# Performance work log

Measured on AMD Instinct MI355X. Metric: run time of the kernel, lower is better.

Reference implementation:

```python
import jax, jax.numpy as jnp
import numpy as np

N = 50000   # nodes
E = 800000  # edges
C = 64      # num_channels
EPS = 1e-5


def setup_inputs() -> dict:
    key = jax.random.key(0)
    ks = jax.random.split(key, 12)
    x = jax.random.normal(ks[0], (N, C), dtype=jnp.float32)
    vec = jax.random.normal(ks[1], (N, 3, C), dtype=jnp.float32)
    senders = jax.random.randint(ks[2], (E,), 0, N, dtype=jnp.int32)
    receivers = jax.random.randint(ks[3], (E,), 0, N, dtype=jnp.int32)
    interaction_matrices = jax.random.normal(ks[4], (E, 3, 3), dtype=jnp.float32)
    # learned parameters
    ln_scale = jnp.ones((C,), dtype=jnp.float32)
    ln_bias = jnp.zeros((C,), dtype=jnp.float32)
    vln_weight = jnp.ones((C,), dtype=jnp.float32)  # VecLayerNorm weight (norm_type='none' -> identity norm, channel scale)
    w1 = jax.random.normal(ks[5], (C, 2 * C), dtype=jnp.float32) / np.sqrt(C)
    b1 = jnp.zeros((2 * C,), dtype=jnp.float32)
    w2 = jax.random.normal(ks[6], (2 * C, C), dtype=jnp.float32) / np.sqrt(2 * C)
    b2 = jnp.zeros((C,), dtype=jnp.float32)
    return {
        "x": x, "vec": vec, "senders": senders, "receivers": receivers,
        "interaction_matrices": interaction_matrices,
        "ln_scale": ln_scale, "ln_bias": ln_bias, "vln_weight": vln_weight,
        "w1": w1, "b1": b1, "w2": w2, "b2": b2,
    }


def reference(x, vec, senders, receivers, interaction_matrices,
              ln_scale, ln_bias, vln_weight, w1, b1, w2, b2):
    # LayerNorm(eps=1e-5) over channel dim
    mean = jnp.mean(x, axis=-1, keepdims=True)
    var = jnp.var(x, axis=-1, keepdims=True)
    x_norm = (x - mean) * jax.lax.rsqrt(var + EPS) * ln_scale + ln_bias
    # VecLayerNorm with norm_type='none': identity norm, learned per-channel weight
    vec_norm = vec * vln_weight  # [N, 3, C]
    # MLP: Dense(2C) -> silu -> Dense(C)
    p = jax.nn.silu(x_norm @ w1 + b1) @ w2 + b2  # [N, C]
    # gather to edges
    p_i = p[receivers]            # [E, C]
    p_j = p[senders]              # [E, C]
    vec_i = vec_norm[receivers]   # [E, 3, C]
    vec_j = vec_norm[senders]     # [E, 3, C]
    source_dipole = p_j[:, None, :] * vec_j                              # [E, 3, C]
    field_at_i = jnp.einsum('eij,ejc->eic', interaction_matrices, source_dipole)  # [E, 3, C]
    dEnergy = jnp.sum(p_i[:, None, :] * vec_i * field_at_i, axis=1)      # [E, C]
    dx = jax.ops.segment_sum(dEnergy, receivers, num_segments=x.shape[0])  # [N, C]
    return dx
```

## Files before the change

kernel.cpp:

```cpp
#include <hip/hip_runtime.h>

#define C 64
#define EPS 1e-5f

typedef __attribute__((ext_vector_type(8))) short bf16x8;
typedef __attribute__((ext_vector_type(4))) float f32x4;

static __device__ __forceinline__ unsigned int f2bf(float f) {
  unsigned int x = __float_as_uint(f);
  return (x + 0x7fffu + ((x >> 16) & 1u)) >> 16;
}
static __device__ __forceinline__ float bflo2f(unsigned int p) {
  return __uint_as_float(p << 16);
}
static __device__ __forceinline__ float bfhi2f(unsigned int p) {
  return __uint_as_float(p & 0xffff0000u);
}

__global__ __launch_bounds__(256) void prep_weights(
    const float* __restrict__ w1, const float* __restrict__ w2,
    unsigned short* __restrict__ w1T, unsigned short* __restrict__ w2T) {
  int idx = blockIdx.x * 256 + threadIdx.x;
  if (idx < 2 * C * C) {
    int k = idx >> 6, c = idx & 63;
    w1T[idx] = (unsigned short)f2bf(w1[c * 2 * C + k]);
  } else if (idx < 4 * C * C) {
    int j = idx - 2 * C * C;
    int c = j >> 7, k = j & 127;
    w2T[j] = (unsigned short)f2bf(w2[k * C + c]);
  }
}

__global__ __launch_bounds__(256, 2) void node_kernel(
    const float* __restrict__ x, const float* __restrict__ vec,
    const float* __restrict__ ln_scale, const float* __restrict__ ln_bias,
    const float* __restrict__ vln_w,
    const unsigned short* __restrict__ w1T, const float* __restrict__ b1,
    const unsigned short* __restrict__ w2T, const float* __restrict__ b2,
    uint2* __restrict__ D16, int n_nodes) {
  __shared__ unsigned short An[64 * 72];
  __shared__ unsigned short Ss[64 * 136];
  __shared__ unsigned short W1s[128 * 72];
  __shared__ unsigned short W2s[64 * 136];

  const int t = threadIdx.x;
  const int lane = t & 63;
  const int wave = t >> 6;
  const int l15 = lane & 15;
  const int q = lane >> 4;

  {
    int r1 = t >> 1, h2 = t & 1;
    const uint4* s1 = (const uint4*)(w1T + r1 * 64 + h2 * 32);
    uint4* d1 = (uint4*)(W1s + r1 * 72 + h2 * 32);
    d1[0] = s1[0]; d1[1] = s1[1]; d1[2] = s1[2]; d1[3] = s1[3];
    int r2 = t >> 2, qd = t & 3;
    const uint4* s2 = (const uint4*)(w2T + r2 * 128 + qd * 32);
    uint4* d2 = (uint4*)(W2s + r2 * 136 + qd * 32);
    d2[0] = s2[0]; d2[1] = s2[1]; d2[2] = s2[2]; d2[3] = s2[3];
  }

  {
    int rowl = t >> 2;
    int part = t & 3;
    int node = blockIdx.x * 64 + rowl;
    int nc = node < n_nodes ? node : n_nodes - 1;
    const float* xp = x + (size_t)nc * C + part * 16;
    float xv[16];
    float s = 0.f;
#pragma unroll
    for (int i = 0; i < 4; i++) {
      float4 v = *(const float4*)(xp + i * 4);
      xv[i * 4 + 0] = v.x; xv[i * 4 + 1] = v.y;
      xv[i * 4 + 2] = v.z; xv[i * 4 + 3] = v.w;
      s += v.x + v.y + v.z + v.w;
    }
    s += __shfl_xor(s, 1);
    s += __shfl_xor(s, 2);
    float mean = s * (1.f / C);
    float vs = 0.f;
#pragma unroll
    for (int i = 0; i < 16; i++) {
      float d = xv[i] - mean;
      vs += d * d;
    }
    vs += __shfl_xor(vs, 1);
    vs += __shfl_xor(vs, 2);
    float rs = rsqrtf(vs * (1.f / C) + EPS);
    float ls[16], lb[16];
#pragma unroll
    for (int i = 0; i < 4; i++) {
      float4 a = *(const float4*)(ln_scale + part * 16 + i * 4);
      float4 b = *(const float4*)(ln_bias + part * 16 + i * 4);
      ls[i * 4 + 0] = a.x; ls[i * 4 + 1] = a.y; ls[i * 4 + 2] = a.z; ls[i * 4 + 3] = a.w;
      lb[i * 4 + 0] = b.x; lb[i * 4 + 1] = b.y; lb[i * 4 + 2] = b.z; lb[i * 4 + 3] = b.w;
    }
    unsigned int bp[8];
#pragma unroll
    for (int i = 0; i < 8; i++) {
      float e0 = (xv[2 * i] - mean) * rs * ls[2 * i] + lb[2 * i];
      float e1 = (xv[2 * i + 1] - mean) * rs * ls[2 * i + 1] + lb[2 * i + 1];
      bp[i] = f2bf(e0) | (f2bf(e1) << 16);
    }
    uint4* dst = (uint4*)(An + rowl * 72 + part * 16);
    uint4 p0 = {bp[0], bp[1], bp[2], bp[3]};
    uint4 p1 = {bp[4], bp[5], bp[6], bp[7]};
    dst[0] = p0;
    dst[1] = p1;
  }
  __syncthreads();

  const int Mbase = wave * 16;

  bf16x8 a0 = *(const bf16x8*)(An + (Mbase + l15) * 72 + q * 8);
  bf16x8 a1 = *(const bf16x8*)(An + (Mbase + l15) * 72 + 32 + q * 8);
  f32x4 acc1[8];
#pragma unroll
  for (int nt = 0; nt < 8; nt++) {
    const unsigned short* wb = W1s + (nt * 16 + l15) * 72 + q * 8;
    bf16x8 b0 = *(const bf16x8*)(wb);
    bf16x8 b1f = *(const bf16x8*)(wb + 32);
    f32x4 z = {0.f, 0.f, 0.f, 0.f};
    z = __builtin_amdgcn_mfma_f32_16x16x32_bf16(a0, b0, z, 0, 0, 0);
    z = __builtin_amdgcn_mfma_f32_16x16x32_bf16(a1, b1f, z, 0, 0, 0);
    acc1[nt] = z;
  }
#pragma unroll
  for (int nt = 0; nt < 8; nt++) {
    float bb = b1[nt * 16 + l15];
#pragma unroll
    for (int r = 0; r < 4; r++) {
      float h = acc1[nt][r] + bb;
      float sg = h / (1.f + __expf(-h));
      Ss[(Mbase + q * 4 + r) * 136 + nt * 16 + l15] = (unsigned short)f2bf(sg);
    }
  }
  __syncthreads();

  bf16x8 a2[4];
#pragma unroll
  for (int kt = 0; kt < 4; kt++)
    a2[kt] = *(const bf16x8*)(Ss + (Mbase + l15) * 136 + kt * 32 + q * 8);
  f32x4 acc2[4];
#pragma unroll
  for (int nt = 0; nt < 4; nt++) {
    f32x4 z = {0.f, 0.f, 0.f, 0.f};
#pragma unroll
    for (int kt = 0; kt < 4; kt++) {
      bf16x8 b = *(const bf16x8*)(W2s + (nt * 16 + l15) * 136 + kt * 32 + q * 8);
      z = __builtin_amdgcn_mfma_f32_16x16x32_bf16(a2[kt], b, z, 0, 0, 0);
    }
    acc2[nt] = z;
  }

#pragma unroll
  for (int nt = 0; nt < 4; nt++) {
    int cc = nt * 16 + l15;
    float bb = b2[cc];
    float vw = vln_w[cc];
#pragma unroll
    for (int r = 0; r < 4; r++) {
      int rl = Mbase + q * 4 + r;
      int nn = blockIdx.x * 64 + rl;
      if (nn < n_nodes) {
        float p = (acc2[nt][r] + bb) * vw;
        const float* vp = vec + (size_t)nn * (3 * C) + cc;
        float v0 = vp[0], v1 = vp[C], v2 = vp[2 * C];
        uint2 u;
        u.x = f2bf(p * v0) | (f2bf(p * v1) << 16);
        u.y = f2bf(p * v2);
        D16[(size_t)nn * C + cc] = u;
      }
    }
  }
}

__global__ __launch_bounds__(256) void edge_kernel(
    const int* __restrict__ senders, const int* __restrict__ receivers,
    const float* __restrict__ Mmat, const uint2* __restrict__ D2,
    float* __restrict__ dx, int n_edges) {
  int wid = threadIdx.x >> 6;
  int lane = threadIdx.x & 63;
  int e0 = (blockIdx.x * 4 + wid) * 4;
  if (e0 >= n_edges) return;
  e0 = __builtin_amdgcn_readfirstlane(e0);
  int nvalid = n_edges - e0;

  int r[4], s[4];
#pragma unroll
  for (int j = 0; j < 4; j++) {
    int e = (j < nvalid) ? e0 + j : e0;
    r[j] = receivers[e];
    s[j] = senders[e];
  }
  uint2 dsv[4], drv[4];
#pragma unroll
  for (int j = 0; j < 4; j++) {
    dsv[j] = D2[(size_t)s[j] * C + lane];
    drv[j] = D2[(size_t)r[j] * C + lane];
  }
#pragma unroll
  for (int j = 0; j < 4; j++) {
    if (j < nvalid) {
      const float* M = Mmat + (size_t)(e0 + j) * 9;
      float m00 = M[0], m01 = M[1], m02 = M[2];
      float m10 = M[3], m11 = M[4], m12 = M[5];
      float m20 = M[6], m21 = M[7], m22 = M[8];
      float s0 = bflo2f(dsv[j].x), s1 = bfhi2f(dsv[j].x), s2 = bflo2f(dsv[j].y);
      float r0 = bflo2f(drv[j].x), r1 = bfhi2f(drv[j].x), r2 = bflo2f(drv[j].y);
      float f0 = m00 * s0 + m01 * s1 + m02 * s2;
      float f1 = m10 * s0 + m11 * s1 + m12 * s2;
      float f2 = m20 * s0 + m21 * s1 + m22 * s2;
      float dE = r0 * f0 + r1 * f1 + r2 * f2;
      atomicAdd(dx + (size_t)r[j] * C + lane, dE);
    }
  }
}

extern "C" void kernel_launch(void* const* d_in, const int* in_sizes, int n_in,
                              void* d_out, int out_size, void* d_ws, size_t ws_size,
                              hipStream_t stream) {
  const float* x        = (const float*)d_in[0];
  const float* vec      = (const float*)d_in[1];
  const int*   senders  = (const int*)d_in[2];
  const int*   receivers= (const int*)d_in[3];
  const float* Mmat     = (const float*)d_in[4];
  const float* ln_scale = (const float*)d_in[5];
  const float* ln_bias  = (const float*)d_in[6];
  const float* vln_w    = (const float*)d_in[7];
  const float* w1       = (const float*)d_in[8];
  const float* b1       = (const float*)d_in[9];
  const float* w2       = (const float*)d_in[10];
  const float* b2       = (const float*)d_in[11];
  float* dx = (float*)d_out;

  int n_nodes = in_sizes[0] / C;
  int n_edges = in_sizes[2];

  unsigned short* w1T = (unsigned short*)d_ws;
  unsigned short* w2T = w1T + 2 * C * C;
  uint2* D16 = (uint2*)((char*)d_ws + 32768);

  prep_weights<<<64, 256, 0, stream>>>(w1, w2, w1T, w2T);

  node_kernel<<<(n_nodes + 63) / 64, 256, 0, stream>>>(
      x, vec, ln_scale, ln_bias, vln_w, w1T, b1, w2T, b2, D16, n_nodes);

  hipMemsetAsync(d_out, 0, (size_t)out_size * sizeof(float), stream);

  edge_kernel<<<(n_edges + 15) / 16, 256, 0, stream>>>(
      senders, receivers, Mmat, D16, dx, n_edges);
}
```

Measured before the change: 323.6 us.

## Replace edge atomics with receiver-sorted CSR gather and per-node accumulation

Builds a CSR grouping of edges by receiver on each call, using a degree histogram, a single-block prefix scan and an atomic scatter. A per-node wave then walks its incoming edges, gathers sender data with one-edge prefetch, and writes dx once with no float atomics or output memset. This removes the atomicAdd contention on dx, at the cost of four extra launches, a serial single-block scan over 50k nodes, and scattered reads of the 3x3 matrices by edge id. Warps also become imbalanced because node degrees vary.

```diff
diff --git a/kernel.cpp b/kernel.cpp
--- a/kernel.cpp
+++ b/kernel.cpp
@@ -28,6 +28,52 @@
     int j = idx - 2 * C * C;
     int c = j >> 7, k = j & 127;
     w2T[j] = (unsigned short)f2bf(w2[k * C + c]);
+  }
+}
+
+__global__ __launch_bounds__(256) void hist_kernel(
+    const int* __restrict__ recv, int* __restrict__ deg, int n_edges) {
+  int i = blockIdx.x * 256 + threadIdx.x;
+  if (i < n_edges) atomicAdd(&deg[recv[i]], 1);
+}
+
+__global__ __launch_bounds__(1024) void scan_kernel(
+    const int* __restrict__ deg, int* __restrict__ off, int* __restrict__ cur,
+    int n_nodes, int n_edges) {
+  __shared__ int part[1024];
+  int tid = threadIdx.x;
+  int chunk = (n_nodes + 1023) / 1024;
+  int b = tid * chunk;
+  int e = b + chunk;
+  if (e > n_nodes) e = n_nodes;
+  int s = 0;
+  for (int i = b; i < e; i++) s += deg[i];
+  part[tid] = s;
+  __syncthreads();
+  for (int d = 1; d < 1024; d <<= 1) {
+    int v = (tid >= d) ? part[tid - d] : 0;
+    __syncthreads();
+    part[tid] += v;
+    __syncthreads();
+  }
+  int run = (tid > 0) ? part[tid - 1] : 0;
+  for (int i = b; i < e; i++) {
+    off[i] = run;
+    cur[i] = run;
+    run += deg[i];
+  }
+  if (tid == 0) off[n_nodes] = n_edges;
+}
+
+__global__ __launch_bounds__(256) void scatter_kernel(
+    const int* __restrict__ send, const int* __restrict__ recv,
+    int* __restrict__ cur, int* __restrict__ sS, int* __restrict__ sE,
+    int n_edges) {
+  int i = blockIdx.x * 256 + threadIdx.x;
+  if (i < n_edges) {
+    int p = atomicAdd(&cur[recv[i]], 1);
+    sS[p] = send[i];
+    sE[p] = i;
   }
 }
 
@@ -175,46 +221,46 @@
   }
 }
 
-__global__ __launch_bounds__(256) void edge_kernel(
-    const int* __restrict__ senders, const int* __restrict__ receivers,
-    const float* __restrict__ Mmat, const uint2* __restrict__ D2,
-    float* __restrict__ dx, int n_edges) {
+__global__ __launch_bounds__(256) void accum_kernel(
+    const int* __restrict__ off, const int* __restrict__ sS,
+    const int* __restrict__ sE, const float* __restrict__ Mmat,
+    const uint2* __restrict__ D2, float* __restrict__ dx, int n_nodes) {
   int wid = threadIdx.x >> 6;
   int lane = threadIdx.x & 63;
-  int e0 = (blockIdx.x * 4 + wid) * 4;
-  if (e0 >= n_edges) return;
-  e0 = __builtin_amdgcn_readfirstlane(e0);
-  int nvalid = n_edges - e0;
-
-  int r[4], s[4];
-#pragma unroll
-  for (int j = 0; j < 4; j++) {
-    int e = (j < nvalid) ? e0 + j : e0;
-    r[j] = receivers[e];
-    s[j] = senders[e];
-  }
-  uint2 dsv[4], drv[4];
-#pragma unroll
-  for (int j = 0; j < 4; j++) {
-    dsv[j] = D2[(size_t)s[j] * C + lane];
-    drv[j] = D2[(size_t)r[j] * C + lane];
-  }
-#pragma unroll
-  for (int j = 0; j < 4; j++) {
-    if (j < nvalid) {
-      const float* M = Mmat + (size_t)(e0 + j) * 9;
-      float m00 = M[0], m01 = M[1], m02 = M[2];
-      float m10 = M[3], m11 = M[4], m12 = M[5];
-      float m20 = M[6], m21 = M[7], m22 = M[8];
-      float s0 = bflo2f(dsv[j].x), s1 = bfhi2f(dsv[j].x), s2 = bflo2f(dsv[j].y);
-      float r0 = bflo2f(drv[j].x), r1 = bfhi2f(drv[j].x), r2 = bflo2f(drv[j].y);
-      float f0 = m00 * s0 + m01 * s1 + m02 * s2;
-      float f1 = m10 * s0 + m11 * s1 + m12 * s2;
-      float f2 = m20 * s0 + m21 * s1 + m22 * s2;
-      float dE = r0 * f0 + r1 * f1 + r2 * f2;
-      atomicAdd(dx + (size_t)r[j] * C + lane, dE);
-    }
-  }
+  int n = blockIdx.x * 4 + wid;
+  if (n >= n_nodes) return;
+
+  int beg = off[n];
+  int end = off[n + 1];
+
+  uint2 dr = D2[(size_t)n * C + lane];
+  float r0 = bflo2f(dr.x), r1 = bfhi2f(dr.x), r2 = bflo2f(dr.y);
+  float acc = 0.f;
+
+  uint2 dsv;
+  int eid = 0;
+  if (beg < end) {
+    dsv = D2[(size_t)sS[beg] * C + lane];
+    eid = sE[beg];
+  }
+  for (int e = beg; e < end; e++) {
+    uint2 cur = dsv;
+    int ce = eid;
+    if (e + 1 < end) {
+      dsv = D2[(size_t)sS[e + 1] * C + lane];
+      eid = sE[e + 1];
+    }
+    const float* M = Mmat + (size_t)__builtin_amdgcn_readfirstlane(ce) * 9;
+    float m00 = M[0], m01 = M[1], m02 = M[2];
+    float m10 = M[3], m11 = M[4], m12 = M[5];
+    float m20 = M[6], m21 = M[7], m22 = M[8];
+    float s0 = bflo2f(cur.x), s1 = bfhi2f(cur.x), s2 = bflo2f(cur.y);
+    float f0 = m00 * s0 + m01 * s1 + m02 * s2;
+    float f1 = m10 * s0 + m11 * s1 + m12 * s2;
+    float f2 = m20 * s0 + m21 * s1 + m22 * s2;
+    acc += r0 * f0 + r1 * f1 + r2 * f2;
+  }
+  dx[(size_t)n * C + lane] = acc;
 }
 
 extern "C" void kernel_launch(void* const* d_in, const int* in_sizes, int n_in,
@@ -240,14 +286,25 @@
   unsigned short* w1T = (unsigned short*)d_ws;
   unsigned short* w2T = w1T + 2 * C * C;
   uint2* D16 = (uint2*)((char*)d_ws + 32768);
+  char* p = (char*)d_ws + 32768 + (size_t)n_nodes * C * sizeof(uint2);
+  p = (char*)(((size_t)p + 255) & ~(size_t)255);
+  int* deg = (int*)p;                 p += (size_t)n_nodes * 4;
+  int* off = (int*)p;                 p += (size_t)(n_nodes + 1) * 4;
+  int* cur = (int*)p;                 p += (size_t)n_nodes * 4;
+  int* sS  = (int*)p;                 p += (size_t)n_edges * 4;
+  int* sE  = (int*)p;
 
   prep_weights<<<64, 256, 0, stream>>>(w1, w2, w1T, w2T);
+
+  hipMemsetAsync(deg, 0, (size_t)n_nodes * 4, stream);
+  hist_kernel<<<(n_edges + 255) / 256, 256, 0, stream>>>(receivers, deg, n_edges);
+  scan_kernel<<<1, 1024, 0, stream>>>(deg, off, cur, n_nodes, n_edges);
+  scatter_kernel<<<(n_edges + 255) / 256, 256, 0, stream>>>(
+      senders, receivers, cur, sS, sE, n_edges);
 
   node_kernel<<<(n_nodes + 63) / 64, 256, 0, stream>>>(
       x, vec, ln_scale, ln_bias, vln_w, w1T, b1, w2T, b2, D16, n_nodes);
 
-  hipMemsetAsync(d_out, 0, (size_t)out_size * sizeof(float), stream);
-
-  edge_kernel<<<(n_edges + 15) / 16, 256, 0, stream>>>(
-      senders, receivers, Mmat, D16, dx, n_edges);
-}
+  accum_kernel<<<(n_nodes + 3) / 4, 256, 0, stream>>>(
+      off, sS, sE, Mmat, D16, dx, n_nodes);
+}
```

After: 451.4 us. 39.5% more time.

## Bin edges by receiver bucket and accumulate in shared memory

Applied to the files above, without the earlier changes.

Adds a binning pass that groups edge indices into 64-node receiver buckets. A per-bucket kernel then accumulates dE in LDS, with receiver rows cached in LDS, and writes dx directly. This replaces global float atomics and the output memset. Buckets that overflow fall back to an overflow list processed with global atomics. The cost is an extra binning kernel, indirect index reads, and loss of coalesced Mmat access.

```diff
diff --git a/kernel.cpp b/kernel.cpp
--- a/kernel.cpp
+++ b/kernel.cpp
@@ -2,6 +2,8 @@
 
 #define C 64
 #define EPS 1e-5f
+#define BUCK_CAP 2048
+#define OVF_CAP 65536
 
 typedef __attribute__((ext_vector_type(8))) short bf16x8;
 typedef __attribute__((ext_vector_type(4))) float f32x4;
@@ -28,6 +30,52 @@
     int j = idx - 2 * C * C;
     int c = j >> 7, k = j & 127;
     w2T[j] = (unsigned short)f2bf(w2[k * C + c]);
+  }
+}
+
+__global__ __launch_bounds__(256) void bin_kernel(
+    const int* __restrict__ recv, int* __restrict__ region,
+    int* __restrict__ bucketCnt, int* __restrict__ ovfList,
+    int* __restrict__ ovfCnt, int n_edges, int nbuck) {
+  __shared__ int hist[1024];
+  int t = threadIdx.x;
+  for (int i = t; i < 1024; i += 256) hist[i] = 0;
+  __syncthreads();
+
+  int base = blockIdx.x * 4096;
+  int mybin[16];
+#pragma unroll 16
+  for (int j = 0; j < 16; j++) {
+    int e = base + j * 256 + t;
+    if (e < n_edges) {
+      int b = recv[e] >> 6;
+      mybin[j] = b;
+      atomicAdd(&hist[b], 1);
+    } else {
+      mybin[j] = -1;
+    }
+  }
+  __syncthreads();
+
+  for (int i = t; i < nbuck; i += 256) {
+    int c = hist[i];
+    hist[i] = (c > 0) ? atomicAdd(&bucketCnt[i], c) : 0;
+  }
+  __syncthreads();
+
+#pragma unroll 16
+  for (int j = 0; j < 16; j++) {
+    int b = mybin[j];
+    if (b >= 0) {
+      int e = base + j * 256 + t;
+      int pos = atomicAdd(&hist[b], 1);
+      if (pos < BUCK_CAP) {
+        region[b * BUCK_CAP + pos] = e;
+      } else {
+        int o = atomicAdd(ovfCnt, 1);
+        if (o < OVF_CAP) ovfList[o] = e;
+      }
+    }
   }
 }
 
@@ -175,45 +223,102 @@
   }
 }
 
-__global__ __launch_bounds__(256) void edge_kernel(
+__global__ __launch_bounds__(256) void accum_bucket(
+    const int* __restrict__ region, const int* __restrict__ bucketCnt,
     const int* __restrict__ senders, const int* __restrict__ receivers,
     const float* __restrict__ Mmat, const uint2* __restrict__ D2,
-    float* __restrict__ dx, int n_edges) {
-  int wid = threadIdx.x >> 6;
+    float* __restrict__ dx, int n_nodes) {
+  __shared__ float acc[64 * 64];
+  __shared__ uint2 rrow[64 * 64];
+  const int b = blockIdx.x;
+  const int node0 = b * 64;
+  const int t = threadIdx.x;
+  const int lane = t & 63;
+  const int wave = t >> 6;
+
+  for (int i = t; i < 4096; i += 256) {
+    acc[i] = 0.f;
+    int row = i >> 6, ln = i & 63;
+    int node = node0 + row;
+    uint2 z; z.x = 0u; z.y = 0u;
+    rrow[i] = (node < n_nodes) ? D2[(size_t)node * C + ln] : z;
+  }
+  __syncthreads();
+
+  int cnt = bucketCnt[b];
+  if (cnt > BUCK_CAP) cnt = BUCK_CAP;
+  const int* reg = region + (size_t)b * BUCK_CAP;
+
+  for (int i = wave * 4; i < cnt; i += 16) {
+    int rem = cnt - i;
+    int i1 = (rem > 1) ? i + 1 : i;
+    int i2 = (rem > 2) ? i + 2 : i;
+    int i3 = (rem > 3) ? i + 3 : i;
+    int e0 = reg[i], e1 = reg[i1], e2 = reg[i2], e3 = reg[i3];
+    int s0 = senders[e0], s1 = senders[e1], s2 = senders[e2], s3 = senders[e3];
+    int r0 = receivers[e0] & 63, r1 = receivers[e1] & 63;
+    int r2 = receivers[e2] & 63, r3 = receivers[e3] & 63;
+    uint2 sv0 = D2[(size_t)s0 * C + lane];
+    uint2 sv1 = D2[(size_t)s1 * C + lane];
+    uint2 sv2 = D2[(size_t)s2 * C + lane];
+    uint2 sv3 = D2[(size_t)s3 * C + lane];
+    uint2 rv0 = rrow[r0 * 64 + lane];
+    uint2 rv1 = rrow[r1 * 64 + lane];
+    uint2 rv2 = rrow[r2 * 64 + lane];
+    uint2 rv3 = rrow[r3 * 64 + lane];
+    const float* M0 = Mmat + (size_t)__builtin_amdgcn_readfirstlane(e0) * 9;
+    const float* M1 = Mmat + (size_t)__builtin_amdgcn_readfirstlane(e1) * 9;
+    const float* M2 = Mmat + (size_t)__builtin_amdgcn_readfirstlane(e2) * 9;
+    const float* M3 = Mmat + (size_t)__builtin_amdgcn_readfirstlane(e3) * 9;
+
+#define EDGE_DOT(J, SV, RV, MP, RR)                                        \
+  if (rem > (J)) {                                                         \
+    float a0 = bflo2f(SV.x), a1 = bfhi2f(SV.x), a2 = bflo2f(SV.y);         \
+    float c0 = bflo2f(RV.x), c1 = bfhi2f(RV.x), c2 = bflo2f(RV.y);         \
+    float f0 = MP[0] * a0 + MP[1] * a1 + MP[2] * a2;                       \
+    float f1 = MP[3] * a0 + MP[4] * a1 + MP[5] * a2;                       \
+    float f2 = MP[6] * a0 + MP[7] * a1 + MP[8] * a2;                       \
+    float dE = c0 * f0 + c1 * f1 + c2 * f2;                                \
+    atomicAdd(&acc[(RR)*64 + lane], dE);                                   \
+  }
+    EDGE_DOT(0, sv0, rv0, M0, r0)
+    EDGE_DOT(1, sv1, rv1, M1, r1)
+    EDGE_DOT(2, sv2, rv2, M2, r2)
+    EDGE_DOT(3, sv3, rv3, M3, r3)
+#undef EDGE_DOT
+  }
+  __syncthreads();
+
+  for (int i = t; i < 4096; i += 256) {
+    int row = i >> 6, ln = i & 63;
+    int node = node0 + row;
+    if (node < n_nodes) dx[(size_t)node * C + ln] = acc[i];
+  }
+}
+
+__global__ __launch_bounds__(256) void fixup_kernel(
+    const int* __restrict__ ovfList, const int* __restrict__ ovfCnt,
+    const int* __restrict__ senders, const int* __restrict__ receivers,
+    const float* __restrict__ Mmat, const uint2* __restrict__ D2,
+    float* __restrict__ dx) {
+  int nov = *ovfCnt;
+  if (nov > OVF_CAP) nov = OVF_CAP;
   int lane = threadIdx.x & 63;
-  int e0 = (blockIdx.x * 4 + wid) * 4;
-  if (e0 >= n_edges) return;
-  e0 = __builtin_amdgcn_readfirstlane(e0);
-  int nvalid = n_edges - e0;
-
-  int r[4], s[4];
-#pragma unroll
-  for (int j = 0; j < 4; j++) {
-    int e = (j < nvalid) ? e0 + j : e0;
-    r[j] = receivers[e];
-    s[j] = senders[e];
-  }
-  uint2 dsv[4], drv[4];
-#pragma unroll
-  for (int j = 0; j < 4; j++) {
-    dsv[j] = D2[(size_t)s[j] * C + lane];
-    drv[j] = D2[(size_t)r[j] * C + lane];
-  }
-#pragma unroll
-  for (int j = 0; j < 4; j++) {
-    if (j < nvalid) {
-      const float* M = Mmat + (size_t)(e0 + j) * 9;
-      float m00 = M[0], m01 = M[1], m02 = M[2];
-      float m10 = M[3], m11 = M[4], m12 = M[5];
-      float m20 = M[6], m21 = M[7], m22 = M[8];
-      float s0 = bflo2f(dsv[j].x), s1 = bfhi2f(dsv[j].x), s2 = bflo2f(dsv[j].y);
-      float r0 = bflo2f(drv[j].x), r1 = bfhi2f(drv[j].x), r2 = bflo2f(drv[j].y);
-      float f0 = m00 * s0 + m01 * s1 + m02 * s2;
-      float f1 = m10 * s0 + m11 * s1 + m12 * s2;
-      float f2 = m20 * s0 + m21 * s1 + m22 * s2;
-      float dE = r0 * f0 + r1 * f1 + r2 * f2;
-      atomicAdd(dx + (size_t)r[j] * C + lane, dE);
-    }
+  for (int idx = blockIdx.x * 4 + (threadIdx.x >> 6); idx < nov;
+       idx += gridDim.x * 4) {
+    int e = ovfList[idx];
+    int s = senders[e];
+    int r = receivers[e];
+    uint2 sv = D2[(size_t)s * C + lane];
+    uint2 rv = D2[(size_t)r * C + lane];
+    const float* M = Mmat + (size_t)e * 9;
+    float a0 = bflo2f(sv.x), a1 = bfhi2f(sv.x), a2 = bflo2f(sv.y);
+    float c0 = bflo2f(rv.x), c1 = bfhi2f(rv.x), c2 = bflo2f(rv.y);
+    float f0 = M[0] * a0 + M[1] * a1 + M[2] * a2;
+    float f1 = M[3] * a0 + M[4] * a1 + M[5] * a2;
+    float f2 = M[6] * a0 + M[7] * a1 + M[8] * a2;
+    float dE = c0 * f0 + c1 * f1 + c2 * f2;
+    atomicAdd(dx + (size_t)r * C + lane, dE);
   }
 }
 
@@ -236,18 +341,32 @@
 
   int n_nodes = in_sizes[0] / C;
   int n_edges = in_sizes[2];
+  int nbuck = (n_nodes + 63) >> 6;
 
   unsigned short* w1T = (unsigned short*)d_ws;
   unsigned short* w2T = w1T + 2 * C * C;
   uint2* D16 = (uint2*)((char*)d_ws + 32768);
+  char* p = (char*)d_ws + 32768 + (size_t)n_nodes * C * sizeof(uint2);
+  p = (char*)(((size_t)p + 255) & ~(size_t)255);
+  int* cnts    = (int*)p;  p += (1024 + 1) * 4;
+  p = (char*)(((size_t)p + 255) & ~(size_t)255);
+  int* region  = (int*)p;  p += (size_t)nbuck * BUCK_CAP * 4;
+  int* ovfList = (int*)p;
+  int* bucketCnt = cnts;
+  int* ovfCnt = cnts + 1024;
 
   prep_weights<<<64, 256, 0, stream>>>(w1, w2, w1T, w2T);
+
+  hipMemsetAsync(cnts, 0, (1024 + 1) * sizeof(int), stream);
+  bin_kernel<<<(n_edges + 4095) / 4096, 256, 0, stream>>>(
+      receivers, region, bucketCnt, ovfList, ovfCnt, n_edges, nbuck);
 
   node_kernel<<<(n_nodes + 63) / 64, 256, 0, stream>>>(
       x, vec, ln_scale, ln_bias, vln_w, w1T, b1, w2T, b2, D16, n_nodes);
 
-  hipMemsetAsync(d_out, 0, (size_t)out_size * sizeof(float), stream);
-
-  edge_kernel<<<(n_edges + 15) / 16, 256, 0, stream>>>(
-      senders, receivers, Mmat, D16, dx, n_edges);
-}
+  accum_bucket<<<nbuck, 256, 0, stream>>>(
+      region, bucketCnt, senders, receivers, Mmat, D16, dx, n_nodes);
+
+  fixup_kernel<<<128, 256, 0, stream>>>(
+      ovfList, ovfCnt, senders, receivers, Mmat, D16, dx);
+}
```

Result: slower. 555.8 us (+71.8%).
